# Kernel tuning notes

Hardware: AMD Instinct MI355X
Metric: run time of the kernel (lower is better)

The kernel has to match this reference:

```python
import jax, jax.numpy as jnp
import numpy as np

U, I, D, E = 100000, 50000, 64, 1250000

def setup_inputs() -> dict:
    key = jax.random.key(0)
    k1, k2, k3, k4, k5 = jax.random.split(key, 5)
    return {
        "embed_user": jax.random.normal(k1, (U, D), dtype=jnp.float32),
        "embed_item": jax.random.normal(k2, (I, D), dtype=jnp.float32),
        "edge_vals": jax.random.uniform(k3, (E,), dtype=jnp.float32),
        "u_idx": jax.random.randint(k4, (E,), 0, U),
        "i_idx": jax.random.randint(k5, (E,), 0, I),
    }

def reference(embed_user, embed_item, edge_vals, u_idx, i_idx):
    # user_item_matrix @ X_items : out[u] += w_e * X_items[i_e]   -> [U, D]
    def spmm_ui(x_items):
        return jax.ops.segment_sum(edge_vals[:, None] * x_items[i_idx], u_idx,
                                   num_segments=U)
    # item_user_matrix @ X_users : out[i] += w_e * X_users[u_e]   -> [I, D]
    def spmm_iu(x_users):
        return jax.ops.segment_sum(edge_vals[:, None] * x_users[u_idx], i_idx,
                                   num_segments=I)

    gcn1_users = spmm_ui(embed_item)          # hop 1
    gcn1_items = spmm_iu(embed_user)
    gcn2_users = spmm_ui(gcn1_items)          # hop 2
    gcn2_items = spmm_iu(gcn1_users)
    gcn3_items = spmm_iu(gcn2_users)          # hop 3 (only items path is returned)

    # weighted residual sum: e + 1/2 g1 + 1/3 g2 + 1/4 g3
    gcn_items = embed_item + 0.5 * gcn1_items + (1.0 / 3.0) * gcn2_items + 0.25 * gcn3_items
    return gcn_items
```

## Files before the change

kernel.cpp:

```cpp
#include <hip/hip_runtime.h>

#define U_CNT 100000
#define I_CNT 50000
#define DIM   64
#define E_CNT 1250000

#define NB      256
#define SHIFT_U 9
#define SHIFT_I 8
#define T1      4096
#define EPT1    16
#define CAP_B   8192
#define WQBITS  15
#define CONVB   1024

typedef float floatx2 __attribute__((ext_vector_type(2)));

static __device__ __forceinline__ unsigned short f2bf(float f) {
  unsigned int u = __float_as_uint(f);
  u += 0x7fffu + ((u >> 16) & 1u);
  return (unsigned short)(u >> 16);
}
static __device__ __forceinline__ unsigned int pack_bf2(float x, float y) {
  return (unsigned int)f2bf(x) | ((unsigned int)f2bf(y) << 16);
}
static __device__ __forceinline__ unsigned int pack_fp8x4(float4 a) {
  unsigned int o = __builtin_amdgcn_cvt_pk_fp8_f32(a.x, a.y, 0u, false);
  o = __builtin_amdgcn_cvt_pk_fp8_f32(a.z, a.w, o, true);
  return o;
}

__global__ __launch_bounds__(256) void build_kernel(
    const int* __restrict__ u_idx, const int* __restrict__ i_idx,
    const float* __restrict__ vals,
    int* __restrict__ cursU, int* __restrict__ cursI,
    unsigned int* __restrict__ recsU, unsigned int* __restrict__ recsI,
    unsigned short* __restrict__ dlsU, unsigned short* __restrict__ dlsI,
    const float* __restrict__ embU, unsigned short* __restrict__ ebUb,
    const float* __restrict__ embI, unsigned short* __restrict__ ebIb,
    int E, int p1blocks) {
  __shared__ int histU[NB], histI[NB], lscanU[NB], lscanI[NB], lbaseU[NB], lbaseI[NB];
  __shared__ unsigned int stageU[T1], stageI[T1];
  __shared__ unsigned short dlstU[T1], dlstI[T1];
  __shared__ unsigned char bktU[T1], bktI[T1];
  int t = threadIdx.x;

  if (blockIdx.x >= p1blocks) {
    const int n4U = U_CNT * DIM / 4;
    const int nTot = n4U + I_CNT * DIM / 4;
    for (int i = (blockIdx.x - p1blocks) * 256 + t; i < nTot; i += CONVB * 256) {
      const float* in; unsigned short* outp; int j;
      if (i < n4U) { in = embU; outp = ebUb; j = i; }
      else         { in = embI; outp = ebIb; j = i - n4U; }
      float4 v = ((const float4*)in)[j];
      ushort4 o;
      o.x = f2bf(v.x); o.y = f2bf(v.y); o.z = f2bf(v.z); o.w = f2bf(v.w);
      ((ushort4*)outp)[j] = o;
    }
    return;
  }

  int tile0 = blockIdx.x * T1;
  int cnt = min(T1, E - tile0);

  for (int k = t; k < NB; k += 256) { histU[k] = 0; histI[k] = 0; }
  __syncthreads();

  int du[EPT1], di[EPT1]; unsigned int wq[EPT1];
#pragma unroll
  for (int k = 0; k < EPT1; ++k) {
    int s2 = k * 256 + t;
    if (s2 < cnt) {
      int e = tile0 + s2;
      du[k] = u_idx[e]; di[k] = i_idx[e];
      unsigned int wb = __float_as_uint(vals[e]);
      wq[k] = ((wb + 0x7fffu + ((wb >> 16) & 1u)) >> 16) & 0x7fffu;
      atomicAdd(&histU[du[k] >> SHIFT_U], 1);
      atomicAdd(&histI[di[k] >> SHIFT_I], 1);
    }
  }
  __syncthreads();

  int mU = histU[t], mI = histI[t];
  lbaseU[t] = t * CAP_B + (mU ? atomicAdd(&cursU[t], mU) : 0);
  lbaseI[t] = t * CAP_B + (mI ? atomicAdd(&cursI[t], mI) : 0);
  lscanU[t] = mU; lscanI[t] = mI;
  __syncthreads();
  for (int off = 1; off < NB; off <<= 1) {
    int xu = (t >= off) ? lscanU[t - off] : 0;
    int xi = (t >= off) ? lscanI[t - off] : 0;
    __syncthreads();
    if (t >= off) { lscanU[t] += xu; lscanI[t] += xi; }
    __syncthreads();
  }
  int iU = lscanU[t], iI = lscanI[t];
  __syncthreads();
  lscanU[t] = iU - mU; lscanI[t] = iI - mI;
  histU[t] = 0; histI[t] = 0;
  __syncthreads();

#pragma unroll
  for (int k = 0; k < EPT1; ++k) {
    int s2 = k * 256 + t;
    if (s2 < cnt) {
      int bU = du[k] >> SHIFT_U, bI = di[k] >> SHIFT_I;
      int pU = atomicAdd(&histU[bU], 1);
      int pI = atomicAdd(&histI[bI], 1);
      int sU = lscanU[bU] + pU, sI = lscanI[bI] + pI;
      stageU[sU] = ((unsigned int)di[k] << WQBITS) | wq[k];
      dlstU[sU] = (unsigned short)(du[k] - (bU << SHIFT_U));
      bktU[sU] = (unsigned char)bU;
      stageI[sI] = ((unsigned int)du[k] << WQBITS) | wq[k];
      dlstI[sI] = (unsigned short)(di[k] - (bI << SHIFT_I));
      bktI[sI] = (unsigned char)bI;
    }
  }
  __syncthreads();
  for (int s = t; s < cnt; s += 256) {
    int bU = bktU[s]; int gU = lbaseU[bU] + (s - lscanU[bU]);
    recsU[gU] = stageU[s]; dlsU[gU] = dlstU[s];
    int bI = bktI[s]; int gI = lbaseI[bI] + (s - lscanI[bI]);
    recsI[gI] = stageI[s]; dlsI[gI] = dlstI[s];
  }
}

__global__ __launch_bounds__(256) void csr_finalize_both(
    const int* __restrict__ cursU, const int* __restrict__ cursI,
    unsigned int* __restrict__ recsU, unsigned int* __restrict__ recsI,
    const unsigned short* __restrict__ dlsU, const unsigned short* __restrict__ dlsI,
    int2* __restrict__ rowseU, int2* __restrict__ rowseI, int nbU) {
  __shared__ int rhist[512];
  __shared__ int rscan[512];
  __shared__ int exsc[512];
  __shared__ unsigned int stage[CAP_B];
  int bb = blockIdx.x, t = threadIdx.x;
  const int* curs; unsigned int* recs; const unsigned short* dls; int2* rowse;
  int nrows, shift, b;
  if (bb < nbU) { b = bb; curs = cursU; recs = recsU; dls = dlsU; rowse = rowseU;
                  nrows = U_CNT; shift = SHIFT_U; }
  else          { b = bb - nbU; curs = cursI; recs = recsI; dls = dlsI; rowse = rowseI;
                  nrows = I_CNT; shift = SHIFT_I; }
  int rpb = 1 << shift;
  int start = b * CAP_B;
  int cnt = min(curs[b], CAP_B);
  int rowbase = b << shift;

  for (int k = t; k < rpb; k += 256) rhist[k] = 0;
  __syncthreads();
  for (int s = t; s < cnt; s += 256)
    atomicAdd(&rhist[dls[start + s]], 1);
  __syncthreads();

  for (int k = t; k < rpb; k += 256) rscan[k] = rhist[k];
  __syncthreads();
  for (int off = 1; off < rpb; off <<= 1) {
    int i0 = t, i1 = t + 256;
    int v0 = (i0 < rpb && i0 >= off) ? rscan[i0 - off] : 0;
    int v1 = (i1 < rpb && i1 >= off) ? rscan[i1 - off] : 0;
    __syncthreads();
    if (i0 < rpb && i0 >= off) rscan[i0] += v0;
    if (i1 < rpb && i1 >= off) rscan[i1] += v1;
    __syncthreads();
  }
  for (int k = t; k < rpb; k += 256) exsc[k] = rscan[k] - rhist[k];
  __syncthreads();

  for (int k = t; k < rpb; k += 256) {
    int r = rowbase + k;
    if (r < nrows) rowse[r] = make_int2(start + exsc[k], start + rscan[k]);
  }

  for (int k = t; k < rpb; k += 256) rhist[k] = 0;
  __syncthreads();
  for (int s = t; s < cnt; s += 256) {
    unsigned int rc = recs[start + s];
    int dl = dls[start + s];
    int pos = atomicAdd(&rhist[dl], 1);
    stage[exsc[dl] + pos] = rc;
  }
  __syncthreads();
  for (int s = t; s < cnt; s += 256) recs[start + s] = stage[s];
}


template <int CHUNK>
static __device__ __forceinline__ float4 gather_bf16(
    const unsigned short* __restrict__ sb,
    const unsigned int* __restrict__ recs,
    int start, int end, int sub, int q) {
  const uint2* s64 = (const uint2*)sb;
  constexpr int K = CHUNK / 4;
  float a0 = 0.f, a1 = 0.f, a2 = 0.f, a3 = 0.f;
  for (int p = start; p < end; p += CHUNK) {
    unsigned int r[K]; uint2 v[K];
#pragma unroll
    for (int k = 0; k < K; ++k) {
      int idx = p + 4 * k + q;
      r[k] = (idx < end) ? recs[idx] : 0u;
    }
#pragma unroll
    for (int k = 0; k < K; ++k)
      v[k] = s64[(size_t)(r[k] >> WQBITS) * 16 + sub];
#pragma unroll
    for (int k = 0; k < K; ++k) {
      float w = __uint_as_float((r[k] & 0x7fffu) << 16);
      a0 += w * __uint_as_float(v[k].x << 16);
      a1 += w * __uint_as_float(v[k].x & 0xffff0000u);
      a2 += w * __uint_as_float(v[k].y << 16);
      a3 += w * __uint_as_float(v[k].y & 0xffff0000u);
    }
  }
  a0 += __shfl_xor(a0, 16); a0 += __shfl_xor(a0, 32);
  a1 += __shfl_xor(a1, 16); a1 += __shfl_xor(a1, 32);
  a2 += __shfl_xor(a2, 16); a2 += __shfl_xor(a2, 32);
  a3 += __shfl_xor(a3, 16); a3 += __shfl_xor(a3, 32);
  return make_float4(a0, a1, a2, a3);
}

template <int CHUNK>
static __device__ __forceinline__ void gather_fp8_dual(
    const unsigned int* __restrict__ s1, const unsigned int* __restrict__ s2,
    const unsigned int* __restrict__ recs,
    int start, int end, int sub, int q, float4& o1, float4& o2) {
  constexpr int K = CHUNK / 4;
  float a0 = 0.f, a1 = 0.f, a2 = 0.f, a3 = 0.f;
  float b0 = 0.f, b1 = 0.f, b2 = 0.f, b3 = 0.f;
  for (int p = start; p < end; p += CHUNK) {
    unsigned int r[K], v1[K], v2[K];
#pragma unroll
    for (int k = 0; k < K; ++k) {
      int idx = p + 4 * k + q;
      r[k] = (idx < end) ? recs[idx] : 0u;
    }
#pragma unroll
    for (int k = 0; k < K; ++k) {
      size_t ro = (size_t)(r[k] >> WQBITS) * 16 + sub;
      v1[k] = s1[ro];
      v2[k] = s2[ro];
    }
#pragma unroll
    for (int k = 0; k < K; ++k) {
      float w = __uint_as_float((r[k] & 0x7fffu) << 16);
      floatx2 lo = __builtin_amdgcn_cvt_pk_f32_fp8(v1[k], false);
      floatx2 hi = __builtin_amdgcn_cvt_pk_f32_fp8(v1[k], true);
      a0 += w * lo.x; a1 += w * lo.y; a2 += w * hi.x; a3 += w * hi.y;
      floatx2 lo2 = __builtin_amdgcn_cvt_pk_f32_fp8(v2[k], false);
      floatx2 hi2 = __builtin_amdgcn_cvt_pk_f32_fp8(v2[k], true);
      b0 += w * lo2.x; b1 += w * lo2.y; b2 += w * hi2.x; b3 += w * hi2.y;
    }
  }
  a0 += __shfl_xor(a0, 16); a0 += __shfl_xor(a0, 32);
  a1 += __shfl_xor(a1, 16); a1 += __shfl_xor(a1, 32);
  a2 += __shfl_xor(a2, 16); a2 += __shfl_xor(a2, 32);
  a3 += __shfl_xor(a3, 16); a3 += __shfl_xor(a3, 32);
  b0 += __shfl_xor(b0, 16); b0 += __shfl_xor(b0, 32);
  b1 += __shfl_xor(b1, 16); b1 += __shfl_xor(b1, 32);
  b2 += __shfl_xor(b2, 16); b2 += __shfl_xor(b2, 32);
  b3 += __shfl_xor(b3, 16); b3 += __shfl_xor(b3, 32);
  o1 = make_float4(a0, a1, a2, a3);
  o2 = make_float4(b0, b1, b2, b3);
}

__global__ __launch_bounds__(256) void hop1_kernel(
    const unsigned short* __restrict__ ebU, const unsigned short* __restrict__ ebI,
    const unsigned int* __restrict__ recsU, const int2* __restrict__ rowseU,
    const unsigned int* __restrict__ recsI, const int2* __restrict__ rowseI,
    unsigned int* __restrict__ u1, uint2* __restrict__ i1) {
  int gw = (blockIdx.x * 256 + threadIdx.x) >> 6;
  int lane = threadIdx.x & 63;
  int sub = lane & 15, q = lane >> 4;
  if (gw < U_CNT) {
    int2 se = rowseU[gw];
    float4 a = gather_bf16<16>(ebI, recsU, se.x, se.y, sub, q);
    if (q == 0) u1[(size_t)gw * 16 + sub] = pack_fp8x4(a);
  } else {
    int r = gw - U_CNT;
    if (r >= I_CNT) return;
    int2 se = rowseI[r];
    float4 a = gather_bf16<32>(ebU, recsI, se.x, se.y, sub, q);
    if (q == 0)
      i1[(size_t)r * 16 + sub] = make_uint2(pack_bf2(a.x, a.y), pack_bf2(a.z, a.w));
  }
}

__global__ __launch_bounds__(256) void hop2a_kernel(
    const uint2* __restrict__ i1,
    const unsigned int* __restrict__ recsU, const int2* __restrict__ rowseU,
    unsigned int* __restrict__ u2) {
  int gw = (blockIdx.x * 256 + threadIdx.x) >> 6;
  int lane = threadIdx.x & 63;
  int sub = lane & 15, q = lane >> 4;
  if (gw >= U_CNT) return;
  int2 se = rowseU[gw];
  float4 a = gather_bf16<16>((const unsigned short*)i1, recsU, se.x, se.y, sub, q);
  if (q == 0) u2[(size_t)gw * 16 + sub] = pack_fp8x4(a);
}

__global__ __launch_bounds__(256) void hop2b_kernel(
    const uint2* __restrict__ i1,
    const unsigned int* __restrict__ u1, const unsigned int* __restrict__ u2,
    const unsigned int* __restrict__ recsI, const int2* __restrict__ rowseI,
    const float* __restrict__ e_item, float* __restrict__ out) {
  int gw = (blockIdx.x * 256 + threadIdx.x) >> 6;
  int lane = threadIdx.x & 63;
  int sub = lane & 15, q = lane >> 4;
  if (gw >= I_CNT) return;
  int2 se = rowseI[gw];
  float4 a, b;
  gather_fp8_dual<32>(u1, u2, recsI, se.x, se.y, sub, q, a, b);
  if (q == 0) {
    size_t idx = (size_t)gw * 16 + sub;
    float4 e = ((const float4*)e_item)[idx];
    uint2 ip = i1[idx];
    const float c1 = 0.5f, c2 = (float)(1.0 / 3.0), c3 = 0.25f;
    float4 o;
    o.x = e.x + c1 * __uint_as_float(ip.x << 16)         + c2 * a.x + c3 * b.x;
    o.y = e.y + c1 * __uint_as_float(ip.x & 0xffff0000u) + c2 * a.y + c3 * b.y;
    o.z = e.z + c1 * __uint_as_float(ip.y << 16)         + c2 * a.z + c3 * b.z;
    o.w = e.w + c1 * __uint_as_float(ip.y & 0xffff0000u) + c2 * a.w + c3 * b.w;
    ((float4*)out)[idx] = o;
  }
}

extern "C" void kernel_launch(void* const* d_in, const int* in_sizes, int n_in,
                              void* d_out, int out_size, void* d_ws, size_t ws_size,
                              hipStream_t stream) {
  const float* embed_user = (const float*)d_in[0];
  const float* embed_item = (const float*)d_in[1];
  const float* edge_vals  = (const float*)d_in[2];
  const int*   u_idx      = (const int*)d_in[3];
  const int*   i_idx      = (const int*)d_in[4];
  float* out = (float*)d_out;

  auto align256 = [](size_t x) { return (x + 255) & ~(size_t)255; };
  char* ws = (char*)d_ws;
  size_t off = 0;
  const size_t capRecs = (size_t)NB * CAP_B;
  const size_t uHalf = (size_t)U_CNT * DIM * sizeof(unsigned short);
  const size_t iHalf = (size_t)I_CNT * DIM * sizeof(unsigned short);

  unsigned int* recsU = (unsigned int*)(ws + off); off += align256(capRecs * 4);
  unsigned int* recsI = (unsigned int*)(ws + off); off += align256(capRecs * 4);
  unsigned short* dlU = (unsigned short*)(ws + off);
  unsigned int*   u1b = (unsigned int*)(ws + off);
  off += align256(capRecs * 2);
  unsigned short* dlI = (unsigned short*)(ws + off); off += align256(capRecs * 2);
  unsigned short* ebUb = (unsigned short*)(ws + off); off += align256(uHalf);
  unsigned short* ebIb = (unsigned short*)(ws + off);
  unsigned int*   u2b  = (unsigned int*)(ws + off);
  off += align256(iHalf);
  uint2* i1b = (uint2*)(ws + off); off += align256(iHalf);
  int2* rowseU = (int2*)(ws + off); off += align256((size_t)U_CNT * sizeof(int2));
  int2* rowseI = (int2*)(ws + off); off += align256((size_t)I_CNT * sizeof(int2));
  int* cursU   = (int*)(ws + off);  off += align256(NB * sizeof(int));
  int* cursI   = (int*)(ws + off);  off += align256(NB * sizeof(int));
  (void)ws_size;

  dim3 blk(256);

  hipMemsetAsync(cursU, 0, NB * sizeof(int), stream);
  hipMemsetAsync(cursI, 0, NB * sizeof(int), stream);
  const int p1blocks = (E_CNT + T1 - 1) / T1;
  build_kernel<<<p1blocks + CONVB, blk, 0, stream>>>(
      u_idx, i_idx, edge_vals, cursU, cursI, recsU, recsI, dlU, dlI,
      embed_user, ebUb, embed_item, ebIb, E_CNT, p1blocks);

  const int nbValidU = (U_CNT + (1 << SHIFT_U) - 1) >> SHIFT_U;
  const int nbValidI = (I_CNT + (1 << SHIFT_I) - 1) >> SHIFT_I;
  csr_finalize_both<<<nbValidU + nbValidI, blk, 0, stream>>>(
      cursU, cursI, recsU, recsI, dlU, dlI, rowseU, rowseI, nbValidU);

  const int hopBlocks = (U_CNT + I_CNT + 3) / 4;
  hop1_kernel<<<hopBlocks, blk, 0, stream>>>(ebUb, ebIb, recsU, rowseU,
                                             recsI, rowseI, u1b, i1b);
  hop2a_kernel<<<(U_CNT + 3) / 4, blk, 0, stream>>>(i1b, recsU, rowseU, u2b);
  hop2b_kernel<<<(I_CNT + 3) / 4, blk, 0, stream>>>(i1b, u1b, u2b, recsI, rowseI,
                                                    embed_item, out);
}
```

Measured before the change: 177.3 us.

## Fuse user-side hop1 and hop2 gathers, interleave u1/u2 into one fp8 buffer

```diff
diff --git a/kernel.cpp b/kernel.cpp
--- a/kernel.cpp
+++ b/kernel.cpp
@@ -218,15 +218,17 @@
 }
 
 template <int CHUNK>
-static __device__ __forceinline__ void gather_fp8_dual(
-    const unsigned int* __restrict__ s1, const unsigned int* __restrict__ s2,
+static __device__ __forceinline__ void gather_bf16_dual(
+    const unsigned short* __restrict__ s1, const unsigned short* __restrict__ s2,
     const unsigned int* __restrict__ recs,
     int start, int end, int sub, int q, float4& o1, float4& o2) {
+  const uint2* a64 = (const uint2*)s1;
+  const uint2* b64 = (const uint2*)s2;
   constexpr int K = CHUNK / 4;
   float a0 = 0.f, a1 = 0.f, a2 = 0.f, a3 = 0.f;
   float b0 = 0.f, b1 = 0.f, b2 = 0.f, b3 = 0.f;
   for (int p = start; p < end; p += CHUNK) {
-    unsigned int r[K], v1[K], v2[K];
+    unsigned int r[K]; uint2 v1[K], v2[K];
 #pragma unroll
     for (int k = 0; k < K; ++k) {
       int idx = p + 4 * k + q;
@@ -235,18 +237,20 @@
 #pragma unroll
     for (int k = 0; k < K; ++k) {
       size_t ro = (size_t)(r[k] >> WQBITS) * 16 + sub;
-      v1[k] = s1[ro];
-      v2[k] = s2[ro];
+      v1[k] = a64[ro];
+      v2[k] = b64[ro];
     }
 #pragma unroll
     for (int k = 0; k < K; ++k) {
       float w = __uint_as_float((r[k] & 0x7fffu) << 16);
-      floatx2 lo = __builtin_amdgcn_cvt_pk_f32_fp8(v1[k], false);
-      floatx2 hi = __builtin_amdgcn_cvt_pk_f32_fp8(v1[k], true);
-      a0 += w * lo.x; a1 += w * lo.y; a2 += w * hi.x; a3 += w * hi.y;
-      floatx2 lo2 = __builtin_amdgcn_cvt_pk_f32_fp8(v2[k], false);
-      floatx2 hi2 = __builtin_amdgcn_cvt_pk_f32_fp8(v2[k], true);
-      b0 += w * lo2.x; b1 += w * lo2.y; b2 += w * hi2.x; b3 += w * hi2.y;
+      a0 += w * __uint_as_float(v1[k].x << 16);
+      a1 += w * __uint_as_float(v1[k].x & 0xffff0000u);
+      a2 += w * __uint_as_float(v1[k].y << 16);
+      a3 += w * __uint_as_float(v1[k].y & 0xffff0000u);
+      b0 += w * __uint_as_float(v2[k].x << 16);
+      b1 += w * __uint_as_float(v2[k].x & 0xffff0000u);
+      b2 += w * __uint_as_float(v2[k].y << 16);
+      b3 += w * __uint_as_float(v2[k].y & 0xffff0000u);
     }
   }
   a0 += __shfl_xor(a0, 16); a0 += __shfl_xor(a0, 32);
@@ -261,44 +265,78 @@
   o2 = make_float4(b0, b1, b2, b3);
 }
 
-__global__ __launch_bounds__(256) void hop1_kernel(
-    const unsigned short* __restrict__ ebU, const unsigned short* __restrict__ ebI,
-    const unsigned int* __restrict__ recsU, const int2* __restrict__ rowseU,
+template <int CHUNK>
+static __device__ __forceinline__ void gather_fp8_dual2(
+    const uint2* __restrict__ u12,
+    const unsigned int* __restrict__ recs,
+    int start, int end, int sub, int q, float4& o1, float4& o2) {
+  constexpr int K = CHUNK / 4;
+  float a0 = 0.f, a1 = 0.f, a2 = 0.f, a3 = 0.f;
+  float b0 = 0.f, b1 = 0.f, b2 = 0.f, b3 = 0.f;
+  for (int p = start; p < end; p += CHUNK) {
+    unsigned int r[K]; uint2 v[K];
+#pragma unroll
+    for (int k = 0; k < K; ++k) {
+      int idx = p + 4 * k + q;
+      r[k] = (idx < end) ? recs[idx] : 0u;
+    }
+#pragma unroll
+    for (int k = 0; k < K; ++k)
+      v[k] = u12[(size_t)(r[k] >> WQBITS) * 16 + sub];
+#pragma unroll
+    for (int k = 0; k < K; ++k) {
+      float w = __uint_as_float((r[k] & 0x7fffu) << 16);
+      floatx2 lo = __builtin_amdgcn_cvt_pk_f32_fp8(v[k].x, false);
+      floatx2 hi = __builtin_amdgcn_cvt_pk_f32_fp8(v[k].x, true);
+      a0 += w * lo.x; a1 += w * lo.y; a2 += w * hi.x; a3 += w * hi.y;
+      floatx2 lo2 = __builtin_amdgcn_cvt_pk_f32_fp8(v[k].y, false);
+      floatx2 hi2 = __builtin_amdgcn_cvt_pk_f32_fp8(v[k].y, true);
+      b0 += w * lo2.x; b1 += w * lo2.y; b2 += w * hi2.x; b3 += w * hi2.y;
+    }
+  }
+  a0 += __shfl_xor(a0, 16); a0 += __shfl_xor(a0, 32);
+  a1 += __shfl_xor(a1, 16); a1 += __shfl_xor(a1, 32);
+  a2 += __shfl_xor(a2, 16); a2 += __shfl_xor(a2, 32);
+  a3 += __shfl_xor(a3, 16); a3 += __shfl_xor(a3, 32);
+  b0 += __shfl_xor(b0, 16); b0 += __shfl_xor(b0, 32);
+  b1 += __shfl_xor(b1, 16); b1 += __shfl_xor(b1, 32);
+  b2 += __shfl_xor(b2, 16); b2 += __shfl_xor(b2, 32);
+  b3 += __shfl_xor(b3, 16); b3 += __shfl_xor(b3, 32);
+  o1 = make_float4(a0, a1, a2, a3);
+  o2 = make_float4(b0, b1, b2, b3);
+}
+
+__global__ __launch_bounds__(256) void hop1i_kernel(
+    const unsigned short* __restrict__ ebU,
     const unsigned int* __restrict__ recsI, const int2* __restrict__ rowseI,
-    unsigned int* __restrict__ u1, uint2* __restrict__ i1) {
+    uint2* __restrict__ i1) {
   int gw = (blockIdx.x * 256 + threadIdx.x) >> 6;
   int lane = threadIdx.x & 63;
   int sub = lane & 15, q = lane >> 4;
-  if (gw < U_CNT) {
-    int2 se = rowseU[gw];
-    float4 a = gather_bf16<16>(ebI, recsU, se.x, se.y, sub, q);
-    if (q == 0) u1[(size_t)gw * 16 + sub] = pack_fp8x4(a);
-  } else {
-    int r = gw - U_CNT;
-    if (r >= I_CNT) return;
-    int2 se = rowseI[r];
-    float4 a = gather_bf16<32>(ebU, recsI, se.x, se.y, sub, q);
-    if (q == 0)
-      i1[(size_t)r * 16 + sub] = make_uint2(pack_bf2(a.x, a.y), pack_bf2(a.z, a.w));
-  }
-}
-
-__global__ __launch_bounds__(256) void hop2a_kernel(
-    const uint2* __restrict__ i1,
+  if (gw >= I_CNT) return;
+  int2 se = rowseI[gw];
+  float4 a = gather_bf16<32>(ebU, recsI, se.x, se.y, sub, q);
+  if (q == 0)
+    i1[(size_t)gw * 16 + sub] = make_uint2(pack_bf2(a.x, a.y), pack_bf2(a.z, a.w));
+}
+
+__global__ __launch_bounds__(256) void hop1u_kernel(
+    const unsigned short* __restrict__ ebI, const uint2* __restrict__ i1,
     const unsigned int* __restrict__ recsU, const int2* __restrict__ rowseU,
-    unsigned int* __restrict__ u2) {
+    uint2* __restrict__ u12) {
   int gw = (blockIdx.x * 256 + threadIdx.x) >> 6;
   int lane = threadIdx.x & 63;
   int sub = lane & 15, q = lane >> 4;
   if (gw >= U_CNT) return;
   int2 se = rowseU[gw];
-  float4 a = gather_bf16<16>((const unsigned short*)i1, recsU, se.x, se.y, sub, q);
-  if (q == 0) u2[(size_t)gw * 16 + sub] = pack_fp8x4(a);
+  float4 a, b;
+  gather_bf16_dual<16>(ebI, (const unsigned short*)i1, recsU, se.x, se.y, sub, q, a, b);
+  if (q == 0)
+    u12[(size_t)gw * 16 + sub] = make_uint2(pack_fp8x4(a), pack_fp8x4(b));
 }
 
 __global__ __launch_bounds__(256) void hop2b_kernel(
-    const uint2* __restrict__ i1,
-    const unsigned int* __restrict__ u1, const unsigned int* __restrict__ u2,
+    const uint2* __restrict__ i1, const uint2* __restrict__ u12,
     const unsigned int* __restrict__ recsI, const int2* __restrict__ rowseI,
     const float* __restrict__ e_item, float* __restrict__ out) {
   int gw = (blockIdx.x * 256 + threadIdx.x) >> 6;
@@ -307,7 +345,7 @@
   if (gw >= I_CNT) return;
   int2 se = rowseI[gw];
   float4 a, b;
-  gather_fp8_dual<32>(u1, u2, recsI, se.x, se.y, sub, q, a, b);
+  gather_fp8_dual2<32>(u12, recsI, se.x, se.y, sub, q, a, b);
   if (q == 0) {
     size_t idx = (size_t)gw * 16 + sub;
     float4 e = ((const float4*)e_item)[idx];
@@ -341,25 +379,21 @@
 
   unsigned int* recsU = (unsigned int*)(ws + off); off += align256(capRecs * 4);
   unsigned int* recsI = (unsigned int*)(ws + off); off += align256(capRecs * 4);
-  unsigned short* dlU = (unsigned short*)(ws + off);
-  unsigned int*   u1b = (unsigned int*)(ws + off);
-  off += align256(capRecs * 2);
+  unsigned short* dlU = (unsigned short*)(ws + off); off += align256(capRecs * 2);
   unsigned short* dlI = (unsigned short*)(ws + off); off += align256(capRecs * 2);
   unsigned short* ebUb = (unsigned short*)(ws + off); off += align256(uHalf);
-  unsigned short* ebIb = (unsigned short*)(ws + off);
-  unsigned int*   u2b  = (unsigned int*)(ws + off);
-  off += align256(iHalf);
+  unsigned short* ebIb = (unsigned short*)(ws + off); off += align256(iHalf);
   uint2* i1b = (uint2*)(ws + off); off += align256(iHalf);
+  uint2* u12 = (uint2*)(ws + off); off += align256(uHalf);
   int2* rowseU = (int2*)(ws + off); off += align256((size_t)U_CNT * sizeof(int2));
   int2* rowseI = (int2*)(ws + off); off += align256((size_t)I_CNT * sizeof(int2));
-  int* cursU   = (int*)(ws + off);  off += align256(NB * sizeof(int));
-  int* cursI   = (int*)(ws + off);  off += align256(NB * sizeof(int));
+  int* cursU   = (int*)(ws + off);  off += align256(2 * NB * sizeof(int));
+  int* cursI   = cursU + NB;
   (void)ws_size;
 
   dim3 blk(256);
 
-  hipMemsetAsync(cursU, 0, NB * sizeof(int), stream);
-  hipMemsetAsync(cursI, 0, NB * sizeof(int), stream);
+  hipMemsetAsync(cursU, 0, 2 * NB * sizeof(int), stream);
   const int p1blocks = (E_CNT + T1 - 1) / T1;
   build_kernel<<<p1blocks + CONVB, blk, 0, stream>>>(
       u_idx, i_idx, edge_vals, cursU, cursI, recsU, recsI, dlU, dlI,
@@ -370,10 +404,8 @@
   csr_finalize_both<<<nbValidU + nbValidI, blk, 0, stream>>>(
       cursU, cursI, recsU, recsI, dlU, dlI, rowseU, rowseI, nbValidU);
 
-  const int hopBlocks = (U_CNT + I_CNT + 3) / 4;
-  hop1_kernel<<<hopBlocks, blk, 0, stream>>>(ebUb, ebIb, recsU, rowseU,
-                                             recsI, rowseI, u1b, i1b);
-  hop2a_kernel<<<(U_CNT + 3) / 4, blk, 0, stream>>>(i1b, recsU, rowseU, u2b);
-  hop2b_kernel<<<(I_CNT + 3) / 4, blk, 0, stream>>>(i1b, u1b, u2b, recsI, rowseI,
+  hop1i_kernel<<<(I_CNT + 3) / 4, blk, 0, stream>>>(ebUb, recsI, rowseI, i1b);
+  hop1u_kernel<<<(U_CNT + 3) / 4, blk, 0, stream>>>(ebIb, i1b, recsU, rowseU, u12);
+  hop2b_kernel<<<(I_CNT + 3) / 4, blk, 0, stream>>>(i1b, u12, recsI, rowseI,
                                                     embed_item, out);
 }
```

Result: faster. 147.8 us (-16.6%).
